# Kernel optimization log

Hardware: AMD Instinct MI355X
Metric: run time of the kernel (lower is better)

The kernel has to match this reference:

```python
import jax, jax.numpy as jnp
import numpy as np

B, T, N, E = 8, 12, 10000, 160000
TD, OD = 64, 64  # temporal_dim, output_dim
EPS = 1e-5


def _ln(x, g, b):
    m = jnp.mean(x, axis=-1, keepdims=True)
    v = jnp.var(x, axis=-1, keepdims=True)
    return (x - m) * jax.lax.rsqrt(v + EPS) * g + b


def _gcn_agg(feat, src, dst, n_nodes):
    # feat: [B, N, D]; mean aggregation of src features into dst nodes
    msgs = feat[:, src, :]                                   # [B, E, D]
    deg = jnp.zeros((n_nodes,), feat.dtype).at[dst].add(1.0)  # [N]
    agg = jnp.zeros_like(feat).at[:, dst, :].add(msgs)        # [B, N, D]
    return agg / jnp.maximum(deg, 1.0)[None, :, None]


def setup_inputs() -> dict:
    key = jax.random.key(0)
    ks = jax.random.split(key, 20)
    s = 0.05
    rn = lambda k, shape: jax.random.normal(k, shape, jnp.float32) * s
    return {
        "x": jax.random.normal(ks[0], (B, T, N), jnp.float32),
        "edge_index": jax.random.randint(ks[1], (2, E), 0, N),
        "causal_edge_index": jax.random.randint(ks[2], (2, E), 0, N),
        # temporal branches (Linear over T)
        "W_ht": rn(ks[3], (T, TD)), "b_ht": jnp.zeros((TD,), jnp.float32),
        "W_lt": rn(ks[4], (T, TD)), "b_lt": jnp.zeros((TD,), jnp.float32),
        # high-freq spatial GCN
        "Ws_h": rn(ks[5], (TD, OD)), "Wn_h": rn(ks[6], (TD, OD)), "b_h": jnp.zeros((OD,), jnp.float32),
        # low-freq spatial GCN (base + causal graph)
        "Ws_l": rn(ks[7], (TD, OD)), "Wn_l": rn(ks[8], (TD, OD)), "Wc_l": rn(ks[9], (TD, OD)), "b_l": jnp.zeros((OD,), jnp.float32),
        # residual projections
        "Whr": rn(ks[10], (TD, OD)), "bhr": jnp.zeros((OD,), jnp.float32),
        "Wlr": rn(ks[11], (TD, OD)), "blr": jnp.zeros((OD,), jnp.float32),
        # layer norms
        "g_hn": jnp.ones((OD,), jnp.float32), "b_hn": jnp.zeros((OD,), jnp.float32),
        "g_ln": jnp.ones((OD,), jnp.float32), "b_ln": jnp.zeros((OD,), jnp.float32),
        # attention fusion gate
        "Wa": rn(ks[12], (2 * OD, 2)), "ba": jnp.zeros((2,), jnp.float32),
        # global residual
        "Wg": rn(ks[13], (T, OD)), "bg": jnp.zeros((OD,), jnp.float32),
        "g_gn": jnp.ones((OD,), jnp.float32), "b_gn": jnp.zeros((OD,), jnp.float32),
    }


def reference(x, edge_index, causal_edge_index,
              W_ht, b_ht, W_lt, b_lt,
              Ws_h, Wn_h, b_h, Ws_l, Wn_l, Wc_l, b_l,
              Whr, bhr, Wlr, blr,
              g_hn, b_hn, g_ln, b_ln,
              Wa, ba, Wg, bg, g_gn, b_gn):
    Bx, Tx, Nx = x.shape
    src, dst = edge_index[0], edge_index[1]
    csrc, cdst = causal_edge_index[0], causal_edge_index[1]
    x_for_residual = x + x  # low_src + high_src (both = x in source)

    # --- high-frequency branch ---
    ht = jnp.einsum('btn,td->bnd', x, W_ht) + b_ht          # [B, N, TD]
    agg_h = _gcn_agg(ht, src, dst, Nx)
    high = ht @ Ws_h + agg_h @ Wn_h + b_h                   # [B, N, OD]
    high = high + 0.2 * (ht @ Whr + bhr)
    high = _ln(high, g_hn, b_hn)
    high = jnp.where(high >= 0, high, 0.1 * high)           # leaky_relu(0.1)

    # --- low-frequency branch ---
    lt = jnp.einsum('btn,td->bnd', x, W_lt) + b_lt          # [B, N, TD]
    agg_l = _gcn_agg(lt, src, dst, Nx)
    agg_c = _gcn_agg(lt, csrc, cdst, Nx)
    low = lt @ Ws_l + agg_l @ Wn_l + agg_c @ Wc_l + b_l     # [B, N, OD]
    low = low + 0.2 * (lt @ Wlr + blr)
    low = _ln(low, g_ln, b_ln)
    low = jax.nn.gelu(low, approximate=False)

    # --- attention fusion ---
    logits = jnp.concatenate([high, low], axis=-1) @ Wa + ba  # [B, N, 2]
    a = jax.nn.softmax(logits, axis=-1)
    fused = a[..., 0:1] * high + a[..., 1:2] * low
    fused = fused + 0.3 * high + 0.3 * low

    # --- global residual ---
    residual = jnp.einsum('btn,td->bnd', x_for_residual, Wg) + bg
    residual = _ln(residual, g_gn, b_gn)
    fused = fused + 0.1 * residual

    # return in original [B, output_dim, N] layout
    return (jnp.swapaxes(fused, 1, 2), jnp.swapaxes(high, 1, 2), jnp.swapaxes(low, 1, 2))
```

## Files before the change

kernel.cpp:

```cpp
#include <hip/hip_runtime.h>

#define B_ 8
#define T_ 12
#define N_ 10000
#define E_ 160000
#define NQ_ 24
#define EPS_ 1e-5f
#define CAP_ 64
#define NC32 313
#define NT64 157

#define O_PAR     0
#define O_CURA    24576
#define O_CURC    65536
#define O_SLOTA   106496
#define O_SLOTC   2666496
#define O_XT      5226496

#define P_TAIL 4608

template<int CTRL>
__device__ __forceinline__ float dpp_add(float v) {
    int s = __builtin_amdgcn_update_dpp(0, __float_as_int(v), CTRL, 0xF, 0xF, true);
    return v + __int_as_float(s);
}
__device__ __forceinline__ float wave_sum(float v) {
    v = dpp_add<0x111>(v);
    v = dpp_add<0x112>(v);
    v = dpp_add<0x114>(v);
    v = dpp_add<0x118>(v);
    v = dpp_add<0x142>(v);
    v = dpp_add<0x143>(v);
    return __int_as_float(__builtin_amdgcn_readlane(__float_as_int(v), 63));
}

__device__ __forceinline__ void prep_body(int tid,
    const float* W_ht, const float* b_ht, const float* W_lt, const float* b_lt,
    const float* Ws_h, const float* Wn_h, const float* b_h,
    const float* Ws_l, const float* Wn_l, const float* Wc_l, const float* b_l,
    const float* Whr, const float* bhr, const float* Wlr, const float* blr,
    const float* Wg, float* par)
{
    int t = tid >> 6, d = tid & 63;
    float ah = 0.f, bh = 0.f, al = 0.f, bl = 0.f, cl = 0.f;
    for (int k = 0; k < 64; ++k) {
        float msh = Ws_h[k * 64 + d] + 0.2f * Whr[k * 64 + d];
        float msl = Ws_l[k * 64 + d] + 0.2f * Wlr[k * 64 + d];
        float wht = W_ht[t * 64 + k];
        float wlt = W_lt[t * 64 + k];
        ah += wht * msh;
        bh += wht * Wn_h[k * 64 + d];
        al += wlt * msl;
        bl += wlt * Wn_l[k * 64 + d];
        cl += wlt * Wc_l[k * 64 + d];
    }
    par[d * 72 + 0 * 12 + t] = ah;
    par[d * 72 + 1 * 12 + t] = bh;
    par[d * 72 + 2 * 12 + t] = al;
    par[d * 72 + 3 * 12 + t] = bl;
    par[d * 72 + 4 * 12 + t] = cl;
    par[d * 72 + 5 * 12 + t] = 2.f * Wg[t * 64 + d];

    if (t == 0) {
        float ch0 = b_h[d] + 0.2f * bhr[d];
        float ch1 = 0.f;
        float cl0 = b_l[d] + 0.2f * blr[d];
        float cl1 = 0.f, cl2 = 0.f;
        for (int k = 0; k < 64; ++k) {
            float bht = b_ht[k];
            float blt = b_lt[k];
            float msh = Ws_h[k * 64 + d] + 0.2f * Whr[k * 64 + d];
            float msl = Ws_l[k * 64 + d] + 0.2f * Wlr[k * 64 + d];
            ch0 += bht * msh;
            ch1 += bht * Wn_h[k * 64 + d];
            cl0 += blt * msl;
            cl1 += blt * Wn_l[k * 64 + d];
            cl2 += blt * Wc_l[k * 64 + d];
        }
        par[P_TAIL + 0 * 64 + d] = ch0;
        par[P_TAIL + 1 * 64 + d] = ch1;
        par[P_TAIL + 2 * 64 + d] = cl0;
        par[P_TAIL + 3 * 64 + d] = cl1;
        par[P_TAIL + 4 * 64 + d] = cl2;
    }
}

__global__ __launch_bounds__(256) void k1_kernel(
    const float* __restrict__ x, float* __restrict__ xt,
    const int* __restrict__ ei, const int* __restrict__ cei,
    int* __restrict__ curA, int* __restrict__ curC,
    int* __restrict__ slotA, int* __restrict__ slotC,
    const float* W_ht, const float* b_ht, const float* W_lt, const float* b_lt,
    const float* Ws_h, const float* Wn_h, const float* b_h,
    const float* Ws_l, const float* Wn_l, const float* Wc_l, const float* b_l,
    const float* Whr, const float* bhr, const float* Wlr, const float* blr,
    const float* Wg, float* par)
{
    __shared__ float tld[64 * 98];
    const int tid = threadIdx.x;
    const int blk = blockIdx.x;

    if (blk < NT64) {
        const int n0 = blk * 64;
        const int j = tid & 63;
        const int r0 = tid >> 6;
        const bool ok = (n0 + j) < N_;
#pragma unroll
        for (int rr = 0; rr < 24; ++rr) {
            int r = rr * 4 + r0;
            tld[j * 98 + r] = ok ? x[r * N_ + n0 + j] : 0.f;
        }
        __syncthreads();
        float4* xt4 = (float4*)xt;
#pragma unroll
        for (int it = 0; it < 6; ++it) {
            int idx = it * 256 + tid;
            int jj = idx / 24, q = idx - jj * 24;
            if (n0 + jj < N_) {
                float4 v;
                v.x = tld[jj * 98 + 4 * q + 0];
                v.y = tld[jj * 98 + 4 * q + 1];
                v.z = tld[jj * 98 + 4 * q + 2];
                v.w = tld[jj * 98 + 4 * q + 3];
                xt4[(size_t)(n0 + jj) * NQ_ + q] = v;
            }
        }
        return;
    }
    if (blk == NT64) {
        for (int t = tid; t < 768; t += 256)
            prep_body(t, W_ht, b_ht, W_lt, b_lt, Ws_h, Wn_h, b_h, Ws_l, Wn_l, Wc_l,
                      b_l, Whr, bhr, Wlr, blr, Wg, par);
        return;
    }
    int i = (blk - NT64 - 1) * 256 + tid;
    if (i < E_) {
        int dd = ei[E_ + i];
        int p = atomicAdd(&curA[dd], 1);
        if (p < CAP_) slotA[dd * CAP_ + p] = ei[i];
    } else if (i < 2 * E_) {
        int e = i - E_;
        int dd = cei[E_ + e];
        int p = atomicAdd(&curC[dd], 1);
        if (p < CAP_) slotC[dd * CAP_ + p] = cei[e];
    }
}

__global__ __launch_bounds__(256, 4) void main_kernel(
    const float* __restrict__ x, const float* __restrict__ par,
    const float4* __restrict__ xt4,
    const int* __restrict__ curA, const int* __restrict__ curC,
    const int* __restrict__ slotA, const int* __restrict__ slotC,
    const float* __restrict__ g_hn, const float* __restrict__ b_hn,
    const float* __restrict__ g_ln, const float* __restrict__ b_ln,
    const float* __restrict__ Wa, const float* __restrict__ ba,
    const float* __restrict__ bg, const float* __restrict__ g_gn,
    const float* __restrict__ b_gn,
    float* __restrict__ out)
{
    __shared__ __align__(16) float s_out[3][64 * 33];
    __shared__ __align__(16) float xs[32 * 12];
    __shared__ __align__(16) float as_[32 * 12];
    __shared__ __align__(16) float cs_[32 * 12];
    __shared__ float indA[32];
    __shared__ float indC[32];

    const int tid = threadIdx.x;
    const int lane = tid & 63;
    const int wave = tid >> 6;
    const int b = blockIdx.x & 7;
    const int n0 = (blockIdx.x >> 3) * 32;
    const int d = lane;

    {
        int idx = tid;
        int t = idx >> 5, node = idx & 31;
        int n = n0 + node;
        xs[node * 12 + t] = (n < N_) ? x[(b * T_ + t) * N_ + n] : 0.f;
        idx = tid + 256;
        if (idx < 384) {
            t = idx >> 5; node = idx & 31; n = n0 + node;
            xs[node * 12 + t] = (n < N_) ? x[(b * T_ + t) * N_ + n] : 0.f;
        }
    }

    {
        float4* P4 = (float4*)&s_out[0][0];
        const int p = tid >> 2;
        const int s = tid & 3;
        const int node = p & 31;
        const int set = p >> 5;
        const int n = n0 + node;
        float4 a0 = {0,0,0,0}, a1 = {0,0,0,0}, a2 = {0,0,0,0};
        if (n < N_) {
            const int* sl = (set ? slotC : slotA) + n * CAP_;
            int dgRaw = (set ? curC : curA)[n];
            int dg = dgRaw < CAP_ ? dgRaw : CAP_;
            for (int j = s; j < dg; j += 4) {
                const float4* src = xt4 + (size_t)sl[j] * NQ_ + b * 3;
                float4 v0 = src[0], v1 = src[1], v2 = src[2];
                a0.x += v0.x; a0.y += v0.y; a0.z += v0.z; a0.w += v0.w;
                a1.x += v1.x; a1.y += v1.y; a1.z += v1.z; a1.w += v1.w;
                a2.x += v2.x; a2.y += v2.y; a2.z += v2.z; a2.w += v2.w;
            }
        }
        P4[tid * 3 + 0] = a0;
        P4[tid * 3 + 1] = a1;
        P4[tid * 3 + 2] = a2;
    }
    __syncthreads();
    {
        const float4* P4 = (const float4*)&s_out[0][0];
        if (tid < 192) {
            int p2 = tid / 3, q = tid - p2 * 3;
            int node = p2 & 31, set = p2 >> 5;
            int n = n0 + node;
            float4 s0 = P4[(p2 * 4 + 0) * 3 + q];
            float4 s1 = P4[(p2 * 4 + 1) * 3 + q];
            float4 s2 = P4[(p2 * 4 + 2) * 3 + q];
            float4 s3 = P4[(p2 * 4 + 3) * 3 + q];
            float4 sum;
            sum.x = (s0.x + s1.x) + (s2.x + s3.x);
            sum.y = (s0.y + s1.y) + (s2.y + s3.y);
            sum.z = (s0.z + s1.z) + (s2.z + s3.z);
            sum.w = (s0.w + s1.w) + (s2.w + s3.w);
            int dgRaw = (n < N_) ? (set ? curC : curA)[n] : 0;
            float inv = 1.f / (float)(dgRaw > 0 ? dgRaw : 1);
            sum.x *= inv; sum.y *= inv; sum.z *= inv; sum.w *= inv;
            ((float4*)(set ? cs_ : as_))[node * 3 + q] = sum;
        } else {
            int i = tid - 192;
            int node = i & 31, set = i >> 5;
            int n = n0 + node;
            float f = (n < N_ && (set ? curC : curA)[n] > 0) ? 1.f : 0.f;
            if (set) indC[node] = f; else indA[node] = f;
        }
    }

    float w[72];
    {
        const float4* wv = (const float4*)(par + d * 72);
#pragma unroll
        for (int k = 0; k < 18; ++k) ((float4*)w)[k] = wv[k];
    }
    const float ch0 = par[P_TAIL + 0 * 64 + d], ch1 = par[P_TAIL + 1 * 64 + d];
    const float cl0 = par[P_TAIL + 2 * 64 + d], cl1 = par[P_TAIL + 3 * 64 + d];
    const float cl2 = par[P_TAIL + 4 * 64 + d];
    const float ghn = g_hn[d], bhn = b_hn[d];
    const float gln = g_ln[d], bln = b_ln[d];
    const float ggn = g_gn[d], bgn = b_gn[d];
    const float bgd = bg[d];
    const float wa00 = Wa[d * 2 + 0], wa01 = Wa[d * 2 + 1];
    const float wa10 = Wa[(64 + d) * 2 + 0], wa11 = Wa[(64 + d) * 2 + 1];
    const float ba0 = ba[0], ba1 = ba[1];

    __syncthreads();

#pragma unroll 2
    for (int i = 0; i < 8; ++i) {
        const int nl = wave * 8 + i;
        float u[12], ua[12], uc[12];
#pragma unroll
        for (int k = 0; k < 3; ++k) {
            ((float4*)u)[k]  = ((const float4*)(xs  + nl * 12))[k];
            ((float4*)ua)[k] = ((const float4*)(as_ + nl * 12))[k];
            ((float4*)uc)[k] = ((const float4*)(cs_ + nl * 12))[k];
        }
        const float indd = indA[nl], indc = indC[nl];

        float acc_h = ch0 + indd * ch1;
        float acc_l = cl0 + indd * cl1 + indc * cl2;
        float acc_r = bgd;
#pragma unroll
        for (int t = 0; t < 12; ++t) {
            acc_h += u[t] * w[t]      + ua[t] * w[12 + t];
            acc_l += u[t] * w[24 + t] + ua[t] * w[36 + t] + uc[t] * w[48 + t];
            acc_r += u[t] * w[60 + t];
        }

        float v0 = wave_sum(acc_h);
        float v1 = wave_sum(acc_h * acc_h);
        float v2 = wave_sum(acc_l);
        float v3 = wave_sum(acc_l * acc_l);
        float v4 = wave_sum(acc_r);
        float v5 = wave_sum(acc_r * acc_r);

        const float mh = v0 * (1.f / 64.f);
        const float varh = fmaxf(v1 * (1.f / 64.f) - mh * mh, 0.f);
        float hn = (acc_h - mh) * rsqrtf(varh + EPS_) * ghn + bhn;
        float high = hn >= 0.f ? hn : 0.1f * hn;

        const float ml = v2 * (1.f / 64.f);
        const float varl = fmaxf(v3 * (1.f / 64.f) - ml * ml, 0.f);
        float lnv = (acc_l - ml) * rsqrtf(varl + EPS_) * gln + bln;
        float low = 0.5f * lnv * (1.f + erff(lnv * 0.70710678118654752f));

        const float mr = v4 * (1.f / 64.f);
        const float varr = fmaxf(v5 * (1.f / 64.f) - mr * mr, 0.f);
        float rn = (acc_r - mr) * rsqrtf(varr + EPS_) * ggn + bgn;

        float l0v = wave_sum(high * wa00 + low * wa10);
        float l1v = wave_sum(high * wa01 + low * wa11);
        float a0 = 1.f / (1.f + expf((l1v + ba1) - (l0v + ba0)));
        float fused = a0 * high + (1.f - a0) * low + 0.3f * high + 0.3f * low + 0.1f * rn;

        s_out[0][d * 33 + nl] = fused;
        s_out[1][d * 33 + nl] = high;
        s_out[2][d * 33 + nl] = low;
    }
    __syncthreads();

    const int off1 = B_ * 64 * N_;
    const int off2 = 2 * B_ * 64 * N_;
    for (int e2 = tid; e2 < 64 * 32; e2 += 256) {
        int r = e2 >> 5, nl = e2 & 31;
        int n = n0 + nl;
        if (n < N_) {
            float* o = out + (b * 64 + r) * N_ + n;
            o[0]    = s_out[0][r * 33 + nl];
            o[off1] = s_out[1][r * 33 + nl];
            o[off2] = s_out[2][r * 33 + nl];
        }
    }
}

extern "C" void kernel_launch(void* const* d_in, const int* in_sizes, int n_in,
                              void* d_out, int out_size, void* d_ws, size_t ws_size,
                              hipStream_t stream)
{
    const float* x   = (const float*)d_in[0];
    const int* ei    = (const int*)d_in[1];
    const int* cei   = (const int*)d_in[2];
    const float* W_ht = (const float*)d_in[3];
    const float* b_ht = (const float*)d_in[4];
    const float* W_lt = (const float*)d_in[5];
    const float* b_lt = (const float*)d_in[6];
    const float* Ws_h = (const float*)d_in[7];
    const float* Wn_h = (const float*)d_in[8];
    const float* b_h  = (const float*)d_in[9];
    const float* Ws_l = (const float*)d_in[10];
    const float* Wn_l = (const float*)d_in[11];
    const float* Wc_l = (const float*)d_in[12];
    const float* b_l  = (const float*)d_in[13];
    const float* Whr  = (const float*)d_in[14];
    const float* bhr  = (const float*)d_in[15];
    const float* Wlr  = (const float*)d_in[16];
    const float* blr  = (const float*)d_in[17];
    const float* g_hn = (const float*)d_in[18];
    const float* b_hn = (const float*)d_in[19];
    const float* g_ln = (const float*)d_in[20];
    const float* b_ln = (const float*)d_in[21];
    const float* Wa   = (const float*)d_in[22];
    const float* ba   = (const float*)d_in[23];
    const float* Wg   = (const float*)d_in[24];
    const float* bg   = (const float*)d_in[25];
    const float* g_gn = (const float*)d_in[26];
    const float* b_gn = (const float*)d_in[27];

    char* ws = (char*)d_ws;
    float* par   = (float*)(ws + O_PAR);
    int* curA    = (int*)(ws + O_CURA);
    int* curC    = (int*)(ws + O_CURC);
    int* slotA   = (int*)(ws + O_SLOTA);
    int* slotC   = (int*)(ws + O_SLOTC);
    float* xt    = (float*)(ws + O_XT);

    hipMemsetAsync(ws + O_CURA, 0, O_SLOTA - O_CURA, stream);

    k1_kernel<<<NT64 + 1 + (2 * E_ + 255) / 256, 256, 0, stream>>>(
        x, xt, ei, cei, curA, curC, slotA, slotC,
        W_ht, b_ht, W_lt, b_lt, Ws_h, Wn_h, b_h,
        Ws_l, Wn_l, Wc_l, b_l, Whr, bhr, Wlr, blr, Wg, par);

    main_kernel<<<NC32 * 8, 256, 0, stream>>>(
        x, par, (const float4*)xt, curA, curC, slotA, slotC,
        g_hn, b_hn, g_ln, b_ln, Wa, ba, bg, g_gn, b_gn, (float*)d_out);
}
```

Measured before the change: 223.1 us.

## Split per-node projection into weight phases and vectorize output stores

Splits the per-channel projection loop into three phases (high, low-base, causal plus residual), each loading only its slice of weights. The aim is to reduce live registers at a pinned four waves per EU. It folds the two-way softmax into a single sigmoid over the weight difference, saving one wave reduction per node. It also writes outputs as float4 stores. The tradeoffs are extra __syncthreads, reloading the input vectors from shared memory in each phase, and float4 stores that need N to be a multiple of 4 (10000 is) so that n<N_ holds for each whole vector.

Measured after the change: 823.8 us. +269.3%, slower.

```diff
diff --git a/kernel.cpp b/kernel.cpp
--- a/kernel.cpp
+++ b/kernel.cpp
@@ -146,7 +146,7 @@
     }
 }
 
-__global__ __launch_bounds__(256, 4) void main_kernel(
+__global__ __launch_bounds__(256) __attribute__((amdgpu_waves_per_eu(4, 4))) void main_kernel(
     const float* __restrict__ x, const float* __restrict__ par,
     const float4* __restrict__ xt4,
     const int* __restrict__ curA, const int* __restrict__ curC,
@@ -237,89 +237,152 @@
         }
     }
 
-    float w[72];
-    {
-        const float4* wv = (const float4*)(par + d * 72);
-#pragma unroll
-        for (int k = 0; k < 18; ++k) ((float4*)w)[k] = wv[k];
-    }
-    const float ch0 = par[P_TAIL + 0 * 64 + d], ch1 = par[P_TAIL + 1 * 64 + d];
-    const float cl0 = par[P_TAIL + 2 * 64 + d], cl1 = par[P_TAIL + 3 * 64 + d];
-    const float cl2 = par[P_TAIL + 4 * 64 + d];
-    const float ghn = g_hn[d], bhn = b_hn[d];
-    const float gln = g_ln[d], bln = b_ln[d];
-    const float ggn = g_gn[d], bgn = b_gn[d];
-    const float bgd = bg[d];
-    const float wa00 = Wa[d * 2 + 0], wa01 = Wa[d * 2 + 1];
-    const float wa10 = Wa[(64 + d) * 2 + 0], wa11 = Wa[(64 + d) * 2 + 1];
-    const float ba0 = ba[0], ba1 = ba[1];
-
-    __syncthreads();
-
-#pragma unroll 2
-    for (int i = 0; i < 8; ++i) {
-        const int nl = wave * 8 + i;
-        float u[12], ua[12], uc[12];
-#pragma unroll
-        for (int k = 0; k < 3; ++k) {
-            ((float4*)u)[k]  = ((const float4*)(xs  + nl * 12))[k];
-            ((float4*)ua)[k] = ((const float4*)(as_ + nl * 12))[k];
-            ((float4*)uc)[k] = ((const float4*)(cs_ + nl * 12))[k];
-        }
-        const float indd = indA[nl], indc = indC[nl];
-
-        float acc_h = ch0 + indd * ch1;
-        float acc_l = cl0 + indd * cl1 + indc * cl2;
-        float acc_r = bgd;
-#pragma unroll
-        for (int t = 0; t < 12; ++t) {
-            acc_h += u[t] * w[t]      + ua[t] * w[12 + t];
-            acc_l += u[t] * w[24 + t] + ua[t] * w[36 + t] + uc[t] * w[48 + t];
-            acc_r += u[t] * w[60 + t];
-        }
-
-        float v0 = wave_sum(acc_h);
-        float v1 = wave_sum(acc_h * acc_h);
-        float v2 = wave_sum(acc_l);
-        float v3 = wave_sum(acc_l * acc_l);
-        float v4 = wave_sum(acc_r);
-        float v5 = wave_sum(acc_r * acc_r);
-
-        const float mh = v0 * (1.f / 64.f);
-        const float varh = fmaxf(v1 * (1.f / 64.f) - mh * mh, 0.f);
-        float hn = (acc_h - mh) * rsqrtf(varh + EPS_) * ghn + bhn;
-        float high = hn >= 0.f ? hn : 0.1f * hn;
-
-        const float ml = v2 * (1.f / 64.f);
-        const float varl = fmaxf(v3 * (1.f / 64.f) - ml * ml, 0.f);
-        float lnv = (acc_l - ml) * rsqrtf(varl + EPS_) * gln + bln;
-        float low = 0.5f * lnv * (1.f + erff(lnv * 0.70710678118654752f));
-
-        const float mr = v4 * (1.f / 64.f);
-        const float varr = fmaxf(v5 * (1.f / 64.f) - mr * mr, 0.f);
-        float rn = (acc_r - mr) * rsqrtf(varr + EPS_) * ggn + bgn;
-
-        float l0v = wave_sum(high * wa00 + low * wa10);
-        float l1v = wave_sum(high * wa01 + low * wa11);
-        float a0 = 1.f / (1.f + expf((l1v + ba1) - (l0v + ba0)));
-        float fused = a0 * high + (1.f - a0) * low + 0.3f * high + 0.3f * low + 0.1f * rn;
-
-        s_out[0][d * 33 + nl] = fused;
-        s_out[1][d * 33 + nl] = high;
-        s_out[2][d * 33 + nl] = low;
+    __syncthreads();
+
+    const float4* wv = (const float4*)(par + d * 72);
+    float acch[8], accl[8], accr[8];
+
+    {
+        const float ch0 = par[P_TAIL + 0 * 64 + d];
+        const float ch1 = par[P_TAIL + 1 * 64 + d];
+        float wh[24];
+#pragma unroll
+        for (int k = 0; k < 6; ++k) ((float4*)wh)[k] = wv[k];
+#pragma unroll
+        for (int i = 0; i < 8; ++i) {
+            const int nl = wave * 8 + i;
+            float u[12], ua[12];
+#pragma unroll
+            for (int k = 0; k < 3; ++k) {
+                ((float4*)u)[k]  = ((const float4*)(xs  + nl * 12))[k];
+                ((float4*)ua)[k] = ((const float4*)(as_ + nl * 12))[k];
+            }
+            float h = ch0 + indA[nl] * ch1;
+#pragma unroll
+            for (int t = 0; t < 12; ++t) h += u[t] * wh[t] + ua[t] * wh[12 + t];
+            acch[i] = h;
+        }
+    }
+    __syncthreads();
+
+    {
+        const float cl0 = par[P_TAIL + 2 * 64 + d];
+        const float cl1 = par[P_TAIL + 3 * 64 + d];
+        const float cl2 = par[P_TAIL + 4 * 64 + d];
+        float wl[24];
+#pragma unroll
+        for (int k = 0; k < 6; ++k) ((float4*)wl)[k] = wv[6 + k];
+#pragma unroll
+        for (int i = 0; i < 8; ++i) {
+            const int nl = wave * 8 + i;
+            float u[12], ua[12];
+#pragma unroll
+            for (int k = 0; k < 3; ++k) {
+                ((float4*)u)[k]  = ((const float4*)(xs  + nl * 12))[k];
+                ((float4*)ua)[k] = ((const float4*)(as_ + nl * 12))[k];
+            }
+            float l = cl0 + indA[nl] * cl1 + indC[nl] * cl2;
+#pragma unroll
+            for (int t = 0; t < 12; ++t) l += u[t] * wl[t] + ua[t] * wl[12 + t];
+            accl[i] = l;
+        }
+    }
+    __syncthreads();
+
+    {
+        const float bgd = bg[d];
+        float wc[12], wg_[12];
+#pragma unroll
+        for (int k = 0; k < 3; ++k) ((float4*)wc)[k]  = wv[12 + k];
+#pragma unroll
+        for (int k = 0; k < 3; ++k) ((float4*)wg_)[k] = wv[15 + k];
+#pragma unroll
+        for (int i = 0; i < 8; ++i) {
+            const int nl = wave * 8 + i;
+            float u[12], uc[12];
+#pragma unroll
+            for (int k = 0; k < 3; ++k) {
+                ((float4*)u)[k]  = ((const float4*)(xs  + nl * 12))[k];
+                ((float4*)uc)[k] = ((const float4*)(cs_ + nl * 12))[k];
+            }
+            float l = accl[i];
+            float r = bgd;
+#pragma unroll
+            for (int t = 0; t < 12; ++t) { l += uc[t] * wc[t]; r += u[t] * wg_[t]; }
+            accl[i] = l;
+            accr[i] = r;
+        }
+    }
+    __syncthreads();
+
+    {
+        const float ghn = g_hn[d], bhn = b_hn[d];
+        const float gln = g_ln[d], bln = b_ln[d];
+        const float ggn = g_gn[d], bgn = b_gn[d];
+        const float wd0 = Wa[d * 2 + 0] - Wa[d * 2 + 1];
+        const float wd1 = Wa[(64 + d) * 2 + 0] - Wa[(64 + d) * 2 + 1];
+        const float bad = ba[0] - ba[1];
+#pragma unroll
+        for (int i = 0; i < 8; ++i) {
+            const int nl = wave * 8 + i;
+            const float h = acch[i], l = accl[i], r = accr[i];
+
+            float v0 = wave_sum(h);
+            float v1 = wave_sum(h * h);
+            float v2 = wave_sum(l);
+            float v3 = wave_sum(l * l);
+            float v4 = wave_sum(r);
+            float v5 = wave_sum(r * r);
+
+            const float mh = v0 * (1.f / 64.f);
+            const float varh = fmaxf(v1 * (1.f / 64.f) - mh * mh, 0.f);
+            float hn = (h - mh) * rsqrtf(varh + EPS_) * ghn + bhn;
+            float high = hn >= 0.f ? hn : 0.1f * hn;
+
+            const float ml = v2 * (1.f / 64.f);
+            const float varl = fmaxf(v3 * (1.f / 64.f) - ml * ml, 0.f);
+            float lnv = (l - ml) * rsqrtf(varl + EPS_) * gln + bln;
+            float low = 0.5f * lnv * (1.f + erff(lnv * 0.70710678118654752f));
+
+            const float mr = v4 * (1.f / 64.f);
+            const float varr = fmaxf(v5 * (1.f / 64.f) - mr * mr, 0.f);
+            float rn = (r - mr) * rsqrtf(varr + EPS_) * ggn + bgn;
+
+            float S = wave_sum(high * wd0 + low * wd1);
+            float a0 = 1.f / (1.f + expf(-(S + bad)));
+            float fused = a0 * high + (1.f - a0) * low + 0.3f * high + 0.3f * low + 0.1f * rn;
+
+            s_out[0][d * 33 + nl] = fused;
+            s_out[1][d * 33 + nl] = high;
+            s_out[2][d * 33 + nl] = low;
+        }
     }
     __syncthreads();
 
     const int off1 = B_ * 64 * N_;
     const int off2 = 2 * B_ * 64 * N_;
-    for (int e2 = tid; e2 < 64 * 32; e2 += 256) {
-        int r = e2 >> 5, nl = e2 & 31;
-        int n = n0 + nl;
+#pragma unroll
+    for (int e2 = tid; e2 < 64 * 8; e2 += 256) {
+        int rr = e2 >> 3, q = e2 & 7;
+        int n = n0 + 4 * q;
         if (n < N_) {
-            float* o = out + (b * 64 + r) * N_ + n;
-            o[0]    = s_out[0][r * 33 + nl];
-            o[off1] = s_out[1][r * 33 + nl];
-            o[off2] = s_out[2][r * 33 + nl];
+            float4 o0, o1, o2;
+            o0.x = s_out[0][rr * 33 + 4 * q + 0];
+            o0.y = s_out[0][rr * 33 + 4 * q + 1];
+            o0.z = s_out[0][rr * 33 + 4 * q + 2];
+            o0.w = s_out[0][rr * 33 + 4 * q + 3];
+            o1.x = s_out[1][rr * 33 + 4 * q + 0];
+            o1.y = s_out[1][rr * 33 + 4 * q + 1];
+            o1.z = s_out[1][rr * 33 + 4 * q + 2];
+            o1.w = s_out[1][rr * 33 + 4 * q + 3];
+            o2.x = s_out[2][rr * 33 + 4 * q + 0];
+            o2.y = s_out[2][rr * 33 + 4 * q + 1];
+            o2.z = s_out[2][rr * 33 + 4 * q + 2];
+            o2.w = s_out[2][rr * 33 + 4 * q + 3];
+            float* o = out + (b * 64 + rr) * N_ + n;
+            *(float4*)(o)        = o0;
+            *(float4*)(o + off1) = o1;
+            *(float4*)(o + off2) = o2;
         }
     }
 }
```
